# Optimization experiments

Hardware: AMD Instinct MI355X
Metric: run time of the kernel (lower is better)

Reference implementation:

```python
import jax, jax.numpy as jnp
import numpy as np

N, Q, E, D = 100000, 128, 500000, 32
D4 = 4 * D
RATIO_UPDATE = 0.2
NEG_SLOPE = 0.01  # LeakyReLU default


def setup_inputs() -> dict:
    key = jax.random.key(0)
    ks = jax.random.split(key, 16)
    return {
        "visited_node_score": jax.random.uniform(ks[0], (N,), jnp.float32),
        "node_repr": jax.random.normal(ks[1], (N, D), jnp.float32),
        "eg0": jnp.sort(jax.random.randint(ks[2], (E,), 0, Q)),
        "src0": jax.random.randint(ks[3], (E,), 0, N),
        "dst0": jax.random.randint(ks[4], (E,), 0, N),
        "rel0": jax.random.normal(ks[5], (E, D), jnp.float32),
        "eg1": jnp.sort(jax.random.randint(ks[6], (E,), 0, Q)),
        "src1": jax.random.randint(ks[7], (E,), 0, N),
        "dst1": jax.random.randint(ks[8], (E,), 0, N),
        "rel1": jax.random.normal(ks[9], (E, D), jnp.float32),
        "query_src_emb": jax.random.normal(ks[10], (Q, D), jnp.float32),
        "query_rel_emb": jax.random.normal(ks[11], (Q, D), jnp.float32),
        "Wq": jax.random.normal(ks[12], (D4, D4), jnp.float32) * np.sqrt(2.0 / D4).astype(np.float32),
        "Wk": jax.random.normal(ks[13], (D4, D4), jnp.float32) * np.sqrt(2.0 / D4).astype(np.float32),
        "Wlin": jax.random.normal(ks[14], (D, D), jnp.float32) * np.sqrt(2.0 / (2 * D)).astype(np.float32),
        "blin": jnp.zeros((D,), jnp.float32),
        "max_edges": 500,
    }


def segment_softmax(logits, seg, num_segments):
    # softmax within groups of identical seg id (source node index)
    m = jax.ops.segment_max(logits, seg, num_segments=num_segments)
    ex = jnp.exp(logits - m[seg])
    s = jax.ops.segment_sum(ex, seg, num_segments=num_segments)
    return ex / s[seg]


def segment_topk_mask(values, seg, k):
    # keep mask for per-segment top-k (seg must be sorted); stable -> first occurrence on ties
    n = values.shape[0]
    order = jnp.lexsort((-values, seg))  # primary: seg, secondary: descending value
    seg_sorted = seg[order]
    idx = jnp.arange(n)
    is_start = jnp.concatenate([jnp.array([True]), seg_sorted[1:] != seg_sorted[:-1]])
    seg_start = jax.lax.cummax(jnp.where(is_start, idx, 0))
    rank_sorted = idx - seg_start  # rank within segment, 0 = largest
    rank = jnp.zeros((n,), jnp.int32).at[order].set(rank_sorted.astype(jnp.int32))
    return rank < k


def reference(visited_node_score, node_repr, eg0, src0, dst0, rel0,
              eg1, src1, dst1, rel1, query_src_emb, query_rel_emb,
              Wq, Wk, Wlin, blin, max_edges):
    def att_logits(repr_, src, dst, eg, rel):
        q = query_src_emb[eg]
        r = query_rel_emb[eg]
        left = jnp.concatenate([repr_[src], rel, q, r], axis=-1)   # [E, 4D]
        right = jnp.concatenate([repr_[dst], rel, q, r], axis=-1)  # [E, 4D]
        return jnp.sum((left @ Wq.T) * (right @ Wk.T), axis=-1)    # [E]

    num_nodes = node_repr.shape[0]

    # ---- last layer: attention + segmented top-k pruning ----
    logits1 = att_logits(node_repr, src1, dst1, eg1, rel1)
    w1 = segment_softmax(logits1, src1, num_nodes)           # softmax over out-edges of each src node
    src_score = visited_node_score[src1]
    target_score = w1 * src_score
    keep = segment_topk_mask(target_score, eg1, max_edges)   # top-k per eg_idx
    w1p = jnp.where(keep, w1, 0.0)

    # node score aggregation == 'sum': score[n] = sum_{kept e: dst=n} w * src_score
    updated_node_score = jax.ops.segment_sum(w1p * src_score, dst1, num_segments=num_nodes)

    # representation update along pruned edges (linear_act=False)
    agg = jax.ops.segment_sum(w1p[:, None] * node_repr[src1], dst1, num_segments=num_nodes)
    repr_ = (1.0 - RATIO_UPDATE) * agg + RATIO_UPDATE * node_repr

    # ---- earlier layer(s), no pruning ----
    logits0 = att_logits(repr_, src0, dst0, eg0, rel0)
    w0 = segment_softmax(logits0, src0, num_nodes)
    agg0 = jax.ops.segment_sum(w0[:, None] * repr_[src0], dst0, num_segments=num_nodes)
    repr_ = (1.0 - RATIO_UPDATE) * agg0 + RATIO_UPDATE * repr_

    # bypass_forward: LeakyReLU(Linear(repr))
    h = repr_ @ Wlin.T + blin
    updated_repr = jnp.where(h >= 0, h, NEG_SLOPE * h)
    return updated_node_score, updated_repr
```

## Files before the change

kernel.cpp:

```cpp
#include <hip/hip_runtime.h>
#include <math.h>

#define DD 32
#define DD4 128
#define TPB 256
#define LDSCAP 6144
#define CANDCAP 2048

__device__ __forceinline__ unsigned long long dsort_key(double x) {
  unsigned long long b = (unsigned long long)__double_as_longlong(x);
  return (b & 0x8000000000000000ull) ? ~b : (b | 0x8000000000000000ull);
}
__device__ __forceinline__ double dunsort_key(unsigned long long k) {
  unsigned long long b = (k & 0x8000000000000000ull) ? (k ^ 0x8000000000000000ull) : ~k;
  return __longlong_as_double((long long)b);
}
__device__ __forceinline__ unsigned int fsort_key(float x) {
  unsigned int b = __float_as_uint(x);
  return (b & 0x80000000u) ? ~b : (b | 0x80000000u);
}
__device__ __forceinline__ float funsort_key(unsigned int k) {
  unsigned int b = (k & 0x80000000u) ? (k ^ 0x80000000u) : ~k;
  return __uint_as_float(b);
}

__device__ __forceinline__ int block_iscan256(int x, int* wsum) {
  const int lane = threadIdx.x & 63, w = threadIdx.x >> 6;
#pragma unroll
  for (int o = 1; o < 64; o <<= 1) {
    int y = __shfl_up(x, o, 64);
    if (lane >= o) x += y;
  }
  if (lane == 63) wsum[w] = x;
  __syncthreads();
  int add = 0;
#pragma unroll
  for (int i = 0; i < 4; ++i) add += (i < w) ? wsum[i] : 0;
  __syncthreads();
  return x + add;
}

__global__ __launch_bounds__(TPB) void k_precompute_M(
    const float* __restrict__ Wq, const float* __restrict__ Wk,
    double* __restrict__ M64, float* __restrict__ M32) {
  int t = blockIdx.x * blockDim.x + threadIdx.x;
  int i = t >> 7, j = t & 127;
  double acc = 0.0;
  for (int k = 0; k < DD4; ++k)
    acc += (double)Wq[k * DD4 + i] * (double)Wk[k * DD4 + j];
  M64[i * DD4 + j] = acc;
  M32[i * DD4 + j] = (float)acc;
}

__global__ __launch_bounds__(TPB) void k_sym22(
    const double* __restrict__ M64, double* __restrict__ S64, float* __restrict__ S32) {
  int i = blockIdx.x * blockDim.x + threadIdx.x;
  int r = i >> 5, c = i & 31;
  double g  = M64[(32 + r) * DD4 + 32 + c];
  double gt = M64[(32 + c) * DD4 + 32 + r];
  double s = (c > r) ? (g + gt) : ((c == r) ? g : 0.0);
  S64[i] = s;
  S32[i] = (float)s;
}

__global__ __launch_bounds__(64) void k_per_query(
    const double* __restrict__ M64,
    const float* __restrict__ qemb, const float* __restrict__ remb,
    double* __restrict__ p64, double* __restrict__ pD64, double* __restrict__ c64,
    float* __restrict__ p32, float* __restrict__ pD32, float* __restrict__ c32) {
  int q = blockIdx.x;
  int l = threadIdx.x;
  __shared__ double qr[64];
  qr[l] = (l < DD) ? (double)qemb[q * DD + l] : (double)remb[q * DD + (l - DD)];
  __syncthreads();
  double a = 0.0;
  for (int j = 0; j < 64; ++j) a += M64[l * DD4 + 64 + j] * qr[j];
  double ct = 0.0;
  for (int j = 0; j < 64; ++j) ct += M64[(64 + j) * DD4 + l] * qr[j];
  if (l >= DD) a += ct;
  p64[q * 64 + l] = a;
  p32[q * 64 + l] = (float)a;
  if (l < DD) {
    pD64[q * DD + l] = ct;
    pD32[q * DD + l] = (float)ct;
  }
  double a3 = 0.0;
  for (int j = 0; j < 64; ++j) a3 += M64[(64 + l) * DD4 + 64 + j] * qr[j];
  a3 *= qr[l];
  for (int o = 32; o; o >>= 1) a3 += __shfl_xor(a3, o);
  if (l == 0) { c64[q] = a3; c32[q] = (float)a3; }
}

#define G_T(c) Mmat[(c) * DD4 + j]
#define G_U(c) Mmat[j * DD4 + 32 + (c)]
#define G_V(c) Mmat[(32 + (c)) * DD4 + j]

#define NP_TILE(GEXPR)                                                          \
  for (int tt = 0; tt < 4; ++tt) {                                              \
    T a0=(T)0,a1=(T)0,a2=(T)0,a3=(T)0,a4=(T)0,a5=(T)0,a6=(T)0,a7=(T)0;          \
    const int c0 = tt * 8;                                                      \
    _Pragma("unroll")                                                           \
    for (int j = 0; j < 32; ++j) {                                              \
      const T hj = hh[j];                                                       \
      a0 += (GEXPR(c0 + 0)) * hj; a1 += (GEXPR(c0 + 1)) * hj;                   \
      a2 += (GEXPR(c0 + 2)) * hj; a3 += (GEXPR(c0 + 3)) * hj;                   \
      a4 += (GEXPR(c0 + 4)) * hj; a5 += (GEXPR(c0 + 5)) * hj;                   \
      a6 += (GEXPR(c0 + 6)) * hj; a7 += (GEXPR(c0 + 7)) * hj;                   \
    }                                                                           \
    xq[tid * 9 + tt * 2]     = make_float4((float)a0,(float)a1,(float)a2,(float)a3); \
    xq[tid * 9 + tt * 2 + 1] = make_float4((float)a4,(float)a5,(float)a6,(float)a7); \
  }

#define NP_STORE(dst)                                                           \
  __syncthreads();                                                              \
  {                                                                             \
    float4* go = (float4*)(dst) + (size_t)nbase * 8;                            \
    _Pragma("unroll")                                                           \
    for (int k = 0; k < 8; ++k) {                                               \
      int f = k * TPB + tid;                                                    \
      if ((f >> 3) < nlim) go[f] = xq[(f >> 3) * 9 + (f & 7)];                  \
    }                                                                           \
  }                                                                             \
  __syncthreads();

template <typename T, bool MIX>
__global__ __launch_bounds__(TPB) void k_node_pre(
    const T* __restrict__ Mmat, const float* __restrict__ reprIn,
    const float* __restrict__ aggIn, float* __restrict__ reprOut,
    float* __restrict__ t, float* __restrict__ u, float* __restrict__ v, int N_) {
  __shared__ float xp[TPB * 36];
  float4* xq = (float4*)xp;
  const int tid = threadIdx.x;
  const int nbase = blockIdx.x * TPB;
  const int n = nbase + tid;
  const int nlim = min(TPB, N_ - nbase);
  const bool valid = tid < nlim;
  T hh[32];
  if (valid) {
    const float4* h4 = (const float4*)reprIn + (size_t)n * 8;
#pragma unroll
    for (int jq = 0; jq < 8; ++jq) {
      float4 x = h4[jq];
      if constexpr (MIX) {
        const float4 a = ((const float4*)aggIn)[(size_t)n * 8 + jq];
        x = make_float4(0.8f * a.x + 0.2f * x.x, 0.8f * a.y + 0.2f * x.y,
                        0.8f * a.z + 0.2f * x.z, 0.8f * a.w + 0.2f * x.w);
        xq[tid * 9 + jq] = x;
      }
      hh[4 * jq]     = (T)x.x; hh[4 * jq + 1] = (T)x.y;
      hh[4 * jq + 2] = (T)x.z; hh[4 * jq + 3] = (T)x.w;
    }
  } else {
#pragma unroll
    for (int j = 0; j < 32; ++j) hh[j] = (T)0;
  }
  if constexpr (MIX) {
    NP_STORE(reprOut)
  }
  NP_TILE(G_T)
  NP_STORE(t)
  NP_TILE(G_U)
  NP_STORE(u)
  NP_TILE(G_V)
  NP_STORE(v)
}

template <typename T>
__global__ __launch_bounds__(TPB) void k_quad(
    const T* __restrict__ Smat,
    const float* __restrict__ rel, const int* __restrict__ eg,
    const T* __restrict__ pq, const T* __restrict__ cq,
    T* __restrict__ quad, int E) {
  const int e = blockIdx.x * TPB + threadIdx.x;
  if (e >= E) return;
  const int q = eg[e];
  T rl[32];
  {
    const float4* r4 = (const float4*)rel + (size_t)e * 8;
#pragma unroll
    for (int j = 0; j < 8; ++j) {
      float4 x = r4[j];
      rl[4 * j] = (T)x.x; rl[4 * j + 1] = (T)x.y;
      rl[4 * j + 2] = (T)x.z; rl[4 * j + 3] = (T)x.w;
    }
  }
  const T* prow = pq + (size_t)q * 64 + 32;
  T lin0 = (T)0, lin1 = (T)0;
#pragma unroll
  for (int i = 0; i < 32; i += 2) {
    lin0 += prow[i] * rl[i];
    lin1 += prow[i + 1] * rl[i + 1];
  }
  T a0 = cq[q] + lin0, a1 = lin1, a2 = (T)0, a3 = (T)0;
#pragma unroll
  for (int i = 0; i < 32; ++i) {
    T r0 = Smat[i * 32 + i] * rl[i];
    T r1 = (T)0;
#pragma unroll
    for (int j = i + 1; j < 32; ++j) {
      if ((j - i) & 1) r1 += Smat[i * 32 + j] * rl[j];
      else             r0 += Smat[i * 32 + j] * rl[j];
    }
    T rr = (r0 + r1) * rl[i];
    if ((i & 3) == 0) a0 += rr;
    else if ((i & 3) == 1) a1 += rr;
    else if ((i & 3) == 2) a2 += rr;
    else a3 += rr;
  }
  quad[e] = (a0 + a1) + (a2 + a3);
}

template <typename T>
__global__ __launch_bounds__(TPB) void k_edge_dots(
    const float* __restrict__ repr, const float* __restrict__ rel,
    const int* __restrict__ src, const int* __restrict__ dst, const int* __restrict__ eg,
    const float* __restrict__ tvec, const float* __restrict__ uvec, const float* __restrict__ vvec,
    const T* __restrict__ pq, const T* __restrict__ pDq, const T* __restrict__ quad,
    T* __restrict__ logits, void* __restrict__ mkey, int E) {
  const long long t = (long long)blockIdx.x * TPB + threadIdx.x;
  const int e = (int)(t >> 3), part = (int)(t & 7);
  if (e >= E) return;
  const int s = src[e], d = dst[e], q = eg[e];
  const float4 hs = ((const float4*)repr)[(size_t)s * 8 + part];
  const float4 td = ((const float4*)tvec)[(size_t)d * 8 + part];
  const float4 hd = ((const float4*)repr)[(size_t)d * 8 + part];
  const float4 rl = ((const float4*)rel)[(size_t)e * 8 + part];
  const float4 us = ((const float4*)uvec)[(size_t)s * 8 + part];
  const float4 vd = ((const float4*)vvec)[(size_t)d * 8 + part];
  const T* p  = pq  + (size_t)q * 64 + part * 4;
  const T* pD = pDq + (size_t)q * DD + part * 4;
  T a = (T)hs.x * ((T)td.x + p[0]) + (T)hs.y * ((T)td.y + p[1]) +
        (T)hs.z * ((T)td.z + p[2]) + (T)hs.w * ((T)td.w + p[3]);
  a += (T)hd.x * pD[0] + (T)hd.y * pD[1] + (T)hd.z * pD[2] + (T)hd.w * pD[3];
  a += (T)rl.x * (T)(us.x + vd.x) + (T)rl.y * (T)(us.y + vd.y) +
       (T)rl.z * (T)(us.z + vd.z) + (T)rl.w * (T)(us.w + vd.w);
  a += __shfl_xor(a, 1);
  a += __shfl_xor(a, 2);
  a += __shfl_xor(a, 4);
  if (part == 0) {
    a += quad[e];
    logits[e] = a;
    if constexpr (sizeof(T) == 8) {
      atomicMax((unsigned long long*)mkey + s, dsort_key((double)a));
    } else {
      atomicMax((unsigned int*)mkey + s, fsort_key((float)a));
    }
  }
}

__global__ __launch_bounds__(TPB) void k_expsum64(
    double* __restrict__ io, const unsigned long long* __restrict__ mkey,
    const int* __restrict__ src, double* __restrict__ ssum, int E) {
  int e = blockIdx.x * blockDim.x + threadIdx.x;
  if (e >= E) return;
  int s = src[e];
  double ex = exp(io[e] - dunsort_key(mkey[s]));
  io[e] = ex;
  atomicAdd(&ssum[s], ex);
}
__global__ __launch_bounds__(TPB) void k_expsum32h(
    float* __restrict__ io, const unsigned int* __restrict__ mkey,
    const int* __restrict__ src, const int* __restrict__ dst,
    float* __restrict__ ssum, int* __restrict__ cnt, int E) {
  int e = blockIdx.x * blockDim.x + threadIdx.x;
  if (e >= E) return;
  int s = src[e];
  float ex = expf(io[e] - funsort_key(mkey[s]));
  io[e] = ex;
  atomicAdd(&ssum[s], ex);
  atomicAdd(&cnt[dst[e]], 1);
}

__global__ __launch_bounds__(TPB) void k_weights_target(
    const double* __restrict__ ex, const double* __restrict__ ssum,
    const int* __restrict__ src, const float* __restrict__ score,
    const int* __restrict__ eg, int* __restrict__ qoff,
    float* __restrict__ w1f, unsigned int* __restrict__ tkey, int E, int Q) {
  int e = blockIdx.x * blockDim.x + threadIdx.x;
  if (e >= E) return;
  int s = src[e];
  double w = ex[e] / ssum[s];
  float wf = (float)w;
  w1f[e] = wf;
  float tgt = wf * score[s];
  tkey[e] = fsort_key(tgt);
  int cur = eg[e];
  int prev = (e == 0) ? -1 : eg[e - 1];
  for (int v = prev + 1; v <= cur; ++v) qoff[v] = e;
  if (e == E - 1) {
    for (int v = cur + 1; v <= Q; ++v) qoff[v] = E;
  }
}

__global__ __launch_bounds__(TPB) void k_topk(
    const unsigned int* __restrict__ tkey, const float* __restrict__ w1f,
    const int* __restrict__ qoff, const int* __restrict__ maxe,
    float* __restrict__ w1p, int E) {
  __shared__ unsigned int keys[LDSCAP];
  __shared__ int hist[256];
  __shared__ unsigned short cand[CANDCAP];
  __shared__ int wsum[4];
  __shared__ int sh_cnt;
  __shared__ unsigned int sh_prefix;
  __shared__ int sh_need;
  const int q = blockIdx.x;
  const int s = qoff[q], e2 = qoff[q + 1];
  const int n = e2 - s;
  const int K = maxe[0];
  if (n <= K) {
    for (int i = s + threadIdx.x; i < e2; i += TPB) w1p[i] = w1f[i];
    return;
  }
  const bool useLds = (n <= LDSCAP);
  if (useLds) {
    for (int i = threadIdx.x; i < n; i += TPB) keys[i] = tkey[s + i];
  }
  hist[threadIdx.x] = 0;
  __syncthreads();
  for (int i = threadIdx.x; i < n; i += TPB) {
    unsigned int k = useLds ? keys[i] : tkey[s + i];
    atomicAdd(&hist[k >> 24], 1);
  }
  __syncthreads();
  int need = K;
  {
    int h = hist[255 - threadIdx.x];
    int incl = block_iscan256(h, wsum);
    int excl = incl - h;
    if (incl >= need && excl < need) {
      sh_prefix = (unsigned int)(255 - threadIdx.x) << 24;
      sh_need = need - excl;
    }
  }
  __syncthreads();
  unsigned int prefix = sh_prefix;
  need = sh_need;
  const int cnt0 = hist[prefix >> 24];
  const bool compact = useLds && (cnt0 <= CANDCAP);
  if (threadIdx.x == 0) sh_cnt = 0;
  __syncthreads();
  if (compact) {
    const unsigned int d0 = prefix >> 24;
    for (int i = threadIdx.x; i < n; i += TPB) {
      if ((keys[i] >> 24) == d0) {
        int p = atomicAdd(&sh_cnt, 1);
        cand[p] = (unsigned short)i;
      }
    }
  }
  __syncthreads();
  const int ncand = compact ? sh_cnt : 0;
  for (int pass = 1; pass < 4; ++pass) {
    const int shift = 24 - 8 * pass;
    const unsigned int himask = 0xFFFFFFFFu << (shift + 8);
    hist[threadIdx.x] = 0;
    __syncthreads();
    if (compact) {
      for (int ci = threadIdx.x; ci < ncand; ci += TPB) {
        unsigned int k = keys[cand[ci]];
        if ((k & himask) == prefix) atomicAdd(&hist[(k >> shift) & 255], 1);
      }
    } else {
      for (int i = threadIdx.x; i < n; i += TPB) {
        unsigned int k = useLds ? keys[i] : tkey[s + i];
        if ((k & himask) == prefix) atomicAdd(&hist[(k >> shift) & 255], 1);
      }
    }
    __syncthreads();
    int h = hist[255 - threadIdx.x];
    int incl = block_iscan256(h, wsum);
    int excl = incl - h;
    if (incl >= need && excl < need) {
      sh_prefix = prefix | ((unsigned int)(255 - threadIdx.x) << shift);
      sh_need = need - excl;
    }
    __syncthreads();
    prefix = sh_prefix;
    need = sh_need;
    __syncthreads();
  }
  const unsigned int kth = prefix;
  const int r = need;
  const int C = (n + TPB - 1) / TPB;
  const int b0 = min(threadIdx.x * C, n);
  const int b1 = min(b0 + C, n);
  int myt = 0;
  for (int i = b0; i < b1; ++i) {
    unsigned int k = useLds ? keys[i] : tkey[s + i];
    myt += (k == kth) ? 1 : 0;
  }
  int tincl = block_iscan256(myt, wsum);
  int tiepre = tincl - myt;
  for (int i = b0; i < b1; ++i) {
    unsigned int k = useLds ? keys[i] : tkey[s + i];
    float v = 0.f;
    if (k > kth) {
      v = w1f[s + i];
    } else if (k == kth) {
      if (tiepre < r) v = w1f[s + i];
      ++tiepre;
    }
    w1p[s + i] = v;
  }
}

__global__ __launch_bounds__(TPB) void k_apply1(
    const float* __restrict__ w1p, const int* __restrict__ src, const int* __restrict__ dst,
    const float* __restrict__ repr0, const float* __restrict__ score,
    float* __restrict__ agg, float* __restrict__ score_out, int E) {
  int t = blockIdx.x * blockDim.x + threadIdx.x;
  int e = t >> 3, part = t & 7;
  if (e >= E) return;
  float w = w1p[e];
  if (w == 0.f) return;
  int sv = src[e], dv = dst[e];
  const float4 rv = ((const float4*)repr0)[sv * 8 + part];
  float* ap = agg + (size_t)dv * DD + part * 4;
  atomicAdd(ap + 0, w * rv.x);
  atomicAdd(ap + 1, w * rv.y);
  atomicAdd(ap + 2, w * rv.z);
  atomicAdd(ap + 3, w * rv.w);
  if (part == 0) atomicAdd(score_out + dv, w * score[sv]);
}

#define SCHUNK 1024
__global__ __launch_bounds__(TPB) void k_scan1(
    const int* __restrict__ cnt, int* __restrict__ off, int* __restrict__ bsum, int N_) {
  __shared__ int sd[TPB];
  const int b = blockIdx.x, t = threadIdx.x;
  const int base = b * SCHUNK + t * 4;
  int v[4];
  int s4 = 0;
#pragma unroll
  for (int k = 0; k < 4; ++k) {
    v[k] = (base + k < N_) ? cnt[base + k] : 0;
    s4 += v[k];
  }
  sd[t] = s4;
  __syncthreads();
  for (int o = 1; o < TPB; o <<= 1) {
    int x = (t >= o) ? sd[t - o] : 0;
    __syncthreads();
    sd[t] += x;
    __syncthreads();
  }
  int excl = sd[t] - s4;
  if (t == TPB - 1) bsum[b] = sd[t];
  int run = excl;
#pragma unroll
  for (int k = 0; k < 4; ++k) {
    if (base + k < N_) { off[base + k] = run; run += v[k]; }
  }
}

__global__ __launch_bounds__(TPB) void k_scan2(
    int* __restrict__ bsum, int* __restrict__ off, int nblk, int N_, int E) {
  __shared__ int wsum[4];
  if (nblk <= TPB) {
    int t = threadIdx.x;
    int x = (t < nblk) ? bsum[t] : 0;
    int orig = x;
    const int lane = t & 63, w = t >> 6;
#pragma unroll
    for (int o = 1; o < 64; o <<= 1) {
      int y = __shfl_up(x, o, 64);
      if (lane >= o) x += y;
    }
    if (lane == 63) wsum[w] = x;
    __syncthreads();
    int add = 0;
#pragma unroll
    for (int i = 0; i < 4; ++i) add += (i < w) ? wsum[i] : 0;
    x += add;
    if (t < nblk) bsum[t] = x - orig;
    if (t == 0) off[N_] = E;
  } else {
    if (threadIdx.x != 0) return;
    int run = 0;
    for (int i = 0; i < nblk; ++i) { int tmp = bsum[i]; bsum[i] = run; run += tmp; }
    off[N_] = E;
  }
}

__global__ __launch_bounds__(TPB) void k_scan3(
    int* __restrict__ off, const int* __restrict__ bsum, int* __restrict__ cursor, int N_) {
  int i = blockIdx.x * blockDim.x + threadIdx.x;
  if (i >= N_) return;
  int v = off[i] + bsum[i >> 10];
  off[i] = v;
  cursor[i] = v;
}

__global__ __launch_bounds__(TPB) void k_scatter0(
    const float* __restrict__ ex, const float* __restrict__ ssum,
    const int* __restrict__ src, const int* __restrict__ dst,
    int* __restrict__ cursor, float2* __restrict__ pk, int E) {
  int e = blockIdx.x * blockDim.x + threadIdx.x;
  if (e >= E) return;
  int s = src[e];
  float w = ex[e] / ssum[s];
  int pos = atomicAdd(&cursor[dst[e]], 1);
  pk[pos] = make_float2(w, __int_as_float(s));
}

__global__ __launch_bounds__(TPB) void k_gather_final(
    const float2* __restrict__ pk, const int* __restrict__ off,
    const float* __restrict__ repr1,
    const float* __restrict__ Wlin, const float* __restrict__ blin,
    float* __restrict__ out_repr, int N_) {
  __shared__ float WsT[DD * DD];
  __shared__ float bs[DD];
  for (int i = threadIdx.x; i < DD * DD; i += TPB) {
    int r = i >> 5, c = i & 31;
    WsT[c * DD + r] = Wlin[i];
  }
  if (threadIdx.x < DD) bs[threadIdx.x] = blin[threadIdx.x];
  __syncthreads();
  const int n = blockIdx.x * 8 + (threadIdx.x >> 5);
  const int c = threadIdx.x & 31;
  if (n >= N_) return;
  float acc = 0.f;
  const int j0 = off[n], j1 = off[n + 1];
  for (int base = j0; base < j1; base += 32) {
    const int m = min(32, j1 - base);
    float2 p = (base + c < j1) ? pk[base + c] : make_float2(0.f, 0.f);
    for (int j = 0; j < m; ++j) {
      const float wj = __shfl(p.x, j, 32);
      const int sj = __float_as_int(__shfl(p.y, j, 32));
      acc += wj * repr1[(size_t)sj * DD + c];
    }
  }
  float mix = 0.8f * acc + 0.2f * repr1[(size_t)n * DD + c];
  float o = bs[c];
#pragma unroll 8
  for (int j = 0; j < DD; ++j) {
    float mj = __shfl(mix, j, 32);
    o += WsT[j * DD + c] * mj;
  }
  out_repr[(size_t)n * DD + c] = (o >= 0.f) ? o : 0.01f * o;
}

extern "C" void kernel_launch(void* const* d_in, const int* in_sizes, int n_in,
                              void* d_out, int out_size, void* d_ws, size_t ws_size,
                              hipStream_t stream) {
  (void)n_in; (void)out_size; (void)ws_size;
  const float* score = (const float*)d_in[0];
  const float* nrepr = (const float*)d_in[1];
  const int*   eg0   = (const int*)d_in[2];
  const int*   src0  = (const int*)d_in[3];
  const int*   dst0  = (const int*)d_in[4];
  const float* rel0  = (const float*)d_in[5];
  const int*   eg1   = (const int*)d_in[6];
  const int*   src1  = (const int*)d_in[7];
  const int*   dst1  = (const int*)d_in[8];
  const float* rel1  = (const float*)d_in[9];
  const float* qemb  = (const float*)d_in[10];
  const float* remb  = (const float*)d_in[11];
  const float* Wq    = (const float*)d_in[12];
  const float* Wk    = (const float*)d_in[13];
  const float* Wlin  = (const float*)d_in[14];
  const float* blin  = (const float*)d_in[15];
  const int*   maxe  = (const int*)d_in[16];

  const int N_ = in_sizes[0];
  const int E_ = in_sizes[2];
  const int Q_ = in_sizes[10] / DD;

  char* wsc = (char*)d_ws;
  size_t off = 0;
  auto alloc = [&](size_t bytes) -> void* {
    void* p = wsc + off;
    off += (bytes + 255) & ~(size_t)255;
    return p;
  };
  double* M64  = (double*)alloc((size_t)DD4 * DD4 * 8);
  float*  M32  = (float*)alloc((size_t)DD4 * DD4 * 4);
  double* S64  = (double*)alloc((size_t)DD * DD * 8);
  float*  S32  = (float*)alloc((size_t)DD * DD * 4);
  double* p64  = (double*)alloc((size_t)Q_ * 64 * 8);
  double* pD64 = (double*)alloc((size_t)Q_ * DD * 8);
  double* c64  = (double*)alloc((size_t)Q_ * 8);
  float*  p32  = (float*)alloc((size_t)Q_ * 64 * 4);
  float*  pD32 = (float*)alloc((size_t)Q_ * DD * 4);
  float*  c32  = (float*)alloc((size_t)Q_ * 4);
  int*    qoff = (int*)alloc((size_t)(Q_ + 2) * 4);
  double* lg1  = (double*)alloc((size_t)E_ * 8);
  double* qv64 = (double*)alloc((size_t)E_ * 8);
  float*  w1f  = (float*)alloc((size_t)E_ * 4);
  unsigned int* tkey = (unsigned int*)alloc((size_t)E_ * 4);
  float*  w1p  = (float*)alloc((size_t)E_ * 4);
  float*  lg0  = (float*)alloc((size_t)E_ * 4);
  float*  repr1 = (float*)alloc((size_t)N_ * DD * 4);
  float*  tvec = (float*)alloc((size_t)N_ * DD * 4);
  float*  uvec = (float*)alloc((size_t)N_ * DD * 4);
  float*  vvec = (float*)alloc((size_t)N_ * DD * 4);
  size_t zstart = off;
  unsigned long long* mkey1 = (unsigned long long*)alloc((size_t)N_ * 8);
  double* s1   = (double*)alloc((size_t)N_ * 8);
  float*  agg  = (float*)alloc((size_t)N_ * DD * 4);
  unsigned int* mkey0 = (unsigned int*)alloc((size_t)N_ * 4);
  float*  s0   = (float*)alloc((size_t)N_ * 4);
  size_t zlen = off - zstart;

  float* qv32 = (float*)qv64;

  int* cnt    = (int*)tvec;
  int* offcsr = (int*)tvec + N_;
  int* cursor = (int*)tvec + 2 * (size_t)N_ + 64;
  int* bsum   = (int*)tvec + 3 * (size_t)N_ + 128;
  float2* pk  = (float2*)uvec;

  float* out_score = (float*)d_out;
  float* out_repr  = out_score + N_;

  hipMemsetAsync(wsc + zstart, 0, zlen, stream);
  hipMemsetAsync(d_out, 0, (size_t)N_ * 4, stream);

  k_precompute_M<<<(DD4 * DD4) / TPB, TPB, 0, stream>>>(Wq, Wk, M64, M32);
  k_sym22<<<4, TPB, 0, stream>>>(M64, S64, S32);
  k_per_query<<<Q_, 64, 0, stream>>>(M64, qemb, remb, p64, pD64, c64, p32, pD32, c32);

  const int ngrid = (N_ + TPB - 1) / TPB;
  const int egrid = (E_ + TPB - 1) / TPB;
  const int dgrid = (int)(((size_t)E_ * 8 + TPB - 1) / TPB);

  k_node_pre<double, false><<<ngrid, TPB, 0, stream>>>(M64, nrepr, nullptr, nullptr,
                                                       tvec, uvec, vvec, N_);
  k_quad<double><<<egrid, TPB, 0, stream>>>(S64, rel1, eg1, p64, c64, qv64, E_);
  k_edge_dots<double><<<dgrid, TPB, 0, stream>>>(nrepr, rel1, src1, dst1, eg1,
                                                 tvec, uvec, vvec, p64, pD64, qv64,
                                                 lg1, (void*)mkey1, E_);
  k_expsum64<<<egrid, TPB, 0, stream>>>(lg1, mkey1, src1, s1, E_);
  k_weights_target<<<egrid, TPB, 0, stream>>>(lg1, s1, src1, score, eg1, qoff,
                                              w1f, tkey, E_, Q_);
  k_topk<<<Q_, TPB, 0, stream>>>(tkey, w1f, qoff, maxe, w1p, E_);

  k_apply1<<<dgrid, TPB, 0, stream>>>(w1p, src1, dst1, nrepr, score, agg, out_score, E_);

  k_node_pre<float, true><<<ngrid, TPB, 0, stream>>>(M32, nrepr, agg, repr1,
                                                     tvec, uvec, vvec, N_);
  k_quad<float><<<egrid, TPB, 0, stream>>>(S32, rel0, eg0, p32, c32, qv32, E_);
  k_edge_dots<float><<<dgrid, TPB, 0, stream>>>(repr1, rel0, src0, dst0, eg0,
                                                tvec, uvec, vvec, p32, pD32, qv32,
                                                lg0, (void*)mkey0, E_);

  hipMemsetAsync(cnt, 0, (size_t)N_ * 4, stream);
  k_expsum32h<<<egrid, TPB, 0, stream>>>(lg0, mkey0, src0, dst0, s0, cnt, E_);
  const int nblk = (N_ + SCHUNK - 1) / SCHUNK;
  k_scan1<<<nblk, TPB, 0, stream>>>(cnt, offcsr, bsum, N_);
  k_scan2<<<1, TPB, 0, stream>>>(bsum, offcsr, nblk, N_, E_);
  k_scan3<<<ngrid, TPB, 0, stream>>>(offcsr, bsum, cursor, N_);
  k_scatter0<<<egrid, TPB, 0, stream>>>(lg0, s0, src0, dst0, cursor, pk, E_);
  k_gather_final<<<(N_ + 7) / 8, TPB, 0, stream>>>(pk, offcsr, repr1, Wlin, blin, out_repr, N_);
}
```

Baseline: 644.3 us.

## Process two edges per lane group and split final gather from linear layer

The edge-dot kernel now has each 8-lane group compute logits for two edges, so twice as many independent gathers are in flight per thread and half as many threads are launched. The final stage is split in two. One kernel does the CSR gather with 4-way unrolled independent loads into a mix buffer that reuses vvec. A second kernel applies the 32x32 linear layer and LeakyReLU with one node per thread, writing through shared memory via NP_STORE. The gather-side shuffles go away, at the cost of an extra N×32 buffer round trip through memory and one more launch.

```diff
diff --git a/kernel.cpp b/kernel.cpp
--- a/kernel.cpp
+++ b/kernel.cpp
@@ -218,32 +218,59 @@
     const T* __restrict__ pq, const T* __restrict__ pDq, const T* __restrict__ quad,
     T* __restrict__ logits, void* __restrict__ mkey, int E) {
   const long long t = (long long)blockIdx.x * TPB + threadIdx.x;
-  const int e = (int)(t >> 3), part = (int)(t & 7);
-  if (e >= E) return;
-  const int s = src[e], d = dst[e], q = eg[e];
-  const float4 hs = ((const float4*)repr)[(size_t)s * 8 + part];
-  const float4 td = ((const float4*)tvec)[(size_t)d * 8 + part];
-  const float4 hd = ((const float4*)repr)[(size_t)d * 8 + part];
-  const float4 rl = ((const float4*)rel)[(size_t)e * 8 + part];
-  const float4 us = ((const float4*)uvec)[(size_t)s * 8 + part];
-  const float4 vd = ((const float4*)vvec)[(size_t)d * 8 + part];
-  const T* p  = pq  + (size_t)q * 64 + part * 4;
-  const T* pD = pDq + (size_t)q * DD + part * 4;
-  T a = (T)hs.x * ((T)td.x + p[0]) + (T)hs.y * ((T)td.y + p[1]) +
-        (T)hs.z * ((T)td.z + p[2]) + (T)hs.w * ((T)td.w + p[3]);
-  a += (T)hd.x * pD[0] + (T)hd.y * pD[1] + (T)hd.z * pD[2] + (T)hd.w * pD[3];
-  a += (T)rl.x * (T)(us.x + vd.x) + (T)rl.y * (T)(us.y + vd.y) +
-       (T)rl.z * (T)(us.z + vd.z) + (T)rl.w * (T)(us.w + vd.w);
-  a += __shfl_xor(a, 1);
-  a += __shfl_xor(a, 2);
-  a += __shfl_xor(a, 4);
+  const int part = (int)(t & 7);
+  const int e0 = (int)((t >> 3) * 2);
+  if (e0 >= E) return;
+  const int e1 = e0 + 1;
+  const bool has1 = (e1 < E);
+  const int s0 = src[e0], d0 = dst[e0], q0 = eg[e0];
+  const int s1 = has1 ? src[e1] : s0;
+  const int d1 = has1 ? dst[e1] : d0;
+  const int q1 = has1 ? eg[e1] : q0;
+  const float4* R  = (const float4*)repr;
+  const float4* Tv = (const float4*)tvec;
+  const float4* Uv = (const float4*)uvec;
+  const float4* Vv = (const float4*)vvec;
+  const float4* RL = (const float4*)rel;
+  const float4 hs0 = R[(size_t)s0 * 8 + part],  hs1 = R[(size_t)s1 * 8 + part];
+  const float4 td0 = Tv[(size_t)d0 * 8 + part], td1 = Tv[(size_t)d1 * 8 + part];
+  const float4 hd0 = R[(size_t)d0 * 8 + part],  hd1 = R[(size_t)d1 * 8 + part];
+  const float4 us0 = Uv[(size_t)s0 * 8 + part], us1 = Uv[(size_t)s1 * 8 + part];
+  const float4 vd0 = Vv[(size_t)d0 * 8 + part], vd1 = Vv[(size_t)d1 * 8 + part];
+  const float4 rl0 = RL[(size_t)e0 * 8 + part];
+  const float4 rl1 = has1 ? RL[(size_t)e1 * 8 + part] : rl0;
+  const T* p0  = pq  + (size_t)q0 * 64 + part * 4;
+  const T* p1  = pq  + (size_t)q1 * 64 + part * 4;
+  const T* pD0 = pDq + (size_t)q0 * DD + part * 4;
+  const T* pD1 = pDq + (size_t)q1 * DD + part * 4;
+  T a = (T)hs0.x * ((T)td0.x + p0[0]) + (T)hs0.y * ((T)td0.y + p0[1]) +
+        (T)hs0.z * ((T)td0.z + p0[2]) + (T)hs0.w * ((T)td0.w + p0[3]);
+  a += (T)hd0.x * pD0[0] + (T)hd0.y * pD0[1] + (T)hd0.z * pD0[2] + (T)hd0.w * pD0[3];
+  a += (T)rl0.x * (T)(us0.x + vd0.x) + (T)rl0.y * (T)(us0.y + vd0.y) +
+       (T)rl0.z * (T)(us0.z + vd0.z) + (T)rl0.w * (T)(us0.w + vd0.w);
+  T b = (T)hs1.x * ((T)td1.x + p1[0]) + (T)hs1.y * ((T)td1.y + p1[1]) +
+        (T)hs1.z * ((T)td1.z + p1[2]) + (T)hs1.w * ((T)td1.w + p1[3]);
+  b += (T)hd1.x * pD1[0] + (T)hd1.y * pD1[1] + (T)hd1.z * pD1[2] + (T)hd1.w * pD1[3];
+  b += (T)rl1.x * (T)(us1.x + vd1.x) + (T)rl1.y * (T)(us1.y + vd1.y) +
+       (T)rl1.z * (T)(us1.z + vd1.z) + (T)rl1.w * (T)(us1.w + vd1.w);
+  a += __shfl_xor(a, 1); a += __shfl_xor(a, 2); a += __shfl_xor(a, 4);
+  b += __shfl_xor(b, 1); b += __shfl_xor(b, 2); b += __shfl_xor(b, 4);
   if (part == 0) {
-    a += quad[e];
-    logits[e] = a;
+    a += quad[e0];
+    logits[e0] = a;
     if constexpr (sizeof(T) == 8) {
-      atomicMax((unsigned long long*)mkey + s, dsort_key((double)a));
+      atomicMax((unsigned long long*)mkey + s0, dsort_key((double)a));
     } else {
-      atomicMax((unsigned int*)mkey + s, fsort_key((float)a));
+      atomicMax((unsigned int*)mkey + s0, fsort_key((float)a));
+    }
+    if (has1) {
+      b += quad[e1];
+      logits[e1] = b;
+      if constexpr (sizeof(T) == 8) {
+        atomicMax((unsigned long long*)mkey + s1, dsort_key((double)b));
+      } else {
+        atomicMax((unsigned int*)mkey + s1, fsort_key((float)b));
+      }
     }
   }
 }
@@ -503,41 +530,75 @@
   pk[pos] = make_float2(w, __int_as_float(s));
 }
 
-__global__ __launch_bounds__(TPB) void k_gather_final(
+__global__ __launch_bounds__(TPB) void k_gather_mix(
     const float2* __restrict__ pk, const int* __restrict__ off,
-    const float* __restrict__ repr1,
-    const float* __restrict__ Wlin, const float* __restrict__ blin,
-    float* __restrict__ out_repr, int N_) {
-  __shared__ float WsT[DD * DD];
-  __shared__ float bs[DD];
-  for (int i = threadIdx.x; i < DD * DD; i += TPB) {
-    int r = i >> 5, c = i & 31;
-    WsT[c * DD + r] = Wlin[i];
-  }
-  if (threadIdx.x < DD) bs[threadIdx.x] = blin[threadIdx.x];
-  __syncthreads();
+    const float* __restrict__ repr1, float* __restrict__ mixbuf, int N_) {
   const int n = blockIdx.x * 8 + (threadIdx.x >> 5);
   const int c = threadIdx.x & 31;
   if (n >= N_) return;
+  const float self = repr1[(size_t)n * DD + c];
   float acc = 0.f;
   const int j0 = off[n], j1 = off[n + 1];
-  for (int base = j0; base < j1; base += 32) {
-    const int m = min(32, j1 - base);
-    float2 p = (base + c < j1) ? pk[base + c] : make_float2(0.f, 0.f);
-    for (int j = 0; j < m; ++j) {
-      const float wj = __shfl(p.x, j, 32);
-      const int sj = __float_as_int(__shfl(p.y, j, 32));
-      acc += wj * repr1[(size_t)sj * DD + c];
-    }
-  }
-  float mix = 0.8f * acc + 0.2f * repr1[(size_t)n * DD + c];
-  float o = bs[c];
-#pragma unroll 8
-  for (int j = 0; j < DD; ++j) {
-    float mj = __shfl(mix, j, 32);
-    o += WsT[j * DD + c] * mj;
-  }
-  out_repr[(size_t)n * DD + c] = (o >= 0.f) ? o : 0.01f * o;
+  int j = j0;
+  for (; j + 4 <= j1; j += 4) {
+    const float2 p0 = pk[j], p1 = pk[j + 1], p2 = pk[j + 2], p3 = pk[j + 3];
+    const float g0 = repr1[(size_t)__float_as_int(p0.y) * DD + c];
+    const float g1 = repr1[(size_t)__float_as_int(p1.y) * DD + c];
+    const float g2 = repr1[(size_t)__float_as_int(p2.y) * DD + c];
+    const float g3 = repr1[(size_t)__float_as_int(p3.y) * DD + c];
+    acc += p0.x * g0;
+    acc += p1.x * g1;
+    acc += p2.x * g2;
+    acc += p3.x * g3;
+  }
+  for (; j < j1; ++j) {
+    const float2 p = pk[j];
+    acc += p.x * repr1[(size_t)__float_as_int(p.y) * DD + c];
+  }
+  mixbuf[(size_t)n * DD + c] = 0.8f * acc + 0.2f * self;
+}
+
+__global__ __launch_bounds__(TPB) void k_final_linear(
+    const float* __restrict__ Wlin, const float* __restrict__ blin,
+    const float* __restrict__ mixbuf, float* __restrict__ out_repr, int N_) {
+  __shared__ float xp[TPB * 36];
+  float4* xq = (float4*)xp;
+  const int tid = threadIdx.x;
+  const int nbase = blockIdx.x * TPB;
+  const int n = nbase + tid;
+  const int nlim = min(TPB, N_ - nbase);
+  float m[32];
+  if (tid < nlim) {
+    const float4* h4 = (const float4*)mixbuf + (size_t)n * 8;
+#pragma unroll
+    for (int jq = 0; jq < 8; ++jq) {
+      float4 x = h4[jq];
+      m[4 * jq] = x.x; m[4 * jq + 1] = x.y; m[4 * jq + 2] = x.z; m[4 * jq + 3] = x.w;
+    }
+  } else {
+#pragma unroll
+    for (int j = 0; j < 32; ++j) m[j] = 0.f;
+  }
+  for (int tt = 0; tt < 4; ++tt) {
+    const int c0 = tt * 8;
+    float a0 = blin[c0 + 0], a1 = blin[c0 + 1], a2 = blin[c0 + 2], a3 = blin[c0 + 3];
+    float a4 = blin[c0 + 4], a5 = blin[c0 + 5], a6 = blin[c0 + 6], a7 = blin[c0 + 7];
+#pragma unroll
+    for (int j = 0; j < 32; ++j) {
+      const float hj = m[j];
+      a0 += Wlin[(c0 + 0) * DD + j] * hj; a1 += Wlin[(c0 + 1) * DD + j] * hj;
+      a2 += Wlin[(c0 + 2) * DD + j] * hj; a3 += Wlin[(c0 + 3) * DD + j] * hj;
+      a4 += Wlin[(c0 + 4) * DD + j] * hj; a5 += Wlin[(c0 + 5) * DD + j] * hj;
+      a6 += Wlin[(c0 + 6) * DD + j] * hj; a7 += Wlin[(c0 + 7) * DD + j] * hj;
+    }
+    a0 = (a0 >= 0.f) ? a0 : 0.01f * a0; a1 = (a1 >= 0.f) ? a1 : 0.01f * a1;
+    a2 = (a2 >= 0.f) ? a2 : 0.01f * a2; a3 = (a3 >= 0.f) ? a3 : 0.01f * a3;
+    a4 = (a4 >= 0.f) ? a4 : 0.01f * a4; a5 = (a5 >= 0.f) ? a5 : 0.01f * a5;
+    a6 = (a6 >= 0.f) ? a6 : 0.01f * a6; a7 = (a7 >= 0.f) ? a7 : 0.01f * a7;
+    xq[tid * 9 + tt * 2]     = make_float4(a0, a1, a2, a3);
+    xq[tid * 9 + tt * 2 + 1] = make_float4(a4, a5, a6, a7);
+  }
+  NP_STORE(out_repr)
 }
 
 extern "C" void kernel_launch(void* const* d_in, const int* in_sizes, int n_in,
@@ -609,6 +670,7 @@
   int* cursor = (int*)tvec + 2 * (size_t)N_ + 64;
   int* bsum   = (int*)tvec + 3 * (size_t)N_ + 128;
   float2* pk  = (float2*)uvec;
+  float* mixbuf = vvec;
 
   float* out_score = (float*)d_out;
   float* out_repr  = out_score + N_;
@@ -622,27 +684,28 @@
 
   const int ngrid = (N_ + TPB - 1) / TPB;
   const int egrid = (E_ + TPB - 1) / TPB;
-  const int dgrid = (int)(((size_t)E_ * 8 + TPB - 1) / TPB);
+  const int dgrid1 = (int)(((size_t)E_ * 8 + TPB - 1) / TPB);
+  const int dgrid2 = (int)(((size_t)((E_ + 1) / 2) * 8 + TPB - 1) / TPB);
 
   k_node_pre<double, false><<<ngrid, TPB, 0, stream>>>(M64, nrepr, nullptr, nullptr,
                                                        tvec, uvec, vvec, N_);
   k_quad<double><<<egrid, TPB, 0, stream>>>(S64, rel1, eg1, p64, c64, qv64, E_);
-  k_edge_dots<double><<<dgrid, TPB, 0, stream>>>(nrepr, rel1, src1, dst1, eg1,
-                                                 tvec, uvec, vvec, p64, pD64, qv64,
-                                                 lg1, (void*)mkey1, E_);
+  k_edge_dots<double><<<dgrid2, TPB, 0, stream>>>(nrepr, rel1, src1, dst1, eg1,
+                                                  tvec, uvec, vvec, p64, pD64, qv64,
+                                                  lg1, (void*)mkey1, E_);
   k_expsum64<<<egrid, TPB, 0, stream>>>(lg1, mkey1, src1, s1, E_);
   k_weights_target<<<egrid, TPB, 0, stream>>>(lg1, s1, src1, score, eg1, qoff,
                                               w1f, tkey, E_, Q_);
   k_topk<<<Q_, TPB, 0, stream>>>(tkey, w1f, qoff, maxe, w1p, E_);
 
-  k_apply1<<<dgrid, TPB, 0, stream>>>(w1p, src1, dst1, nrepr, score, agg, out_score, E_);
+  k_apply1<<<dgrid1, TPB, 0, stream>>>(w1p, src1, dst1, nrepr, score, agg, out_score, E_);
 
   k_node_pre<float, true><<<ngrid, TPB, 0, stream>>>(M32, nrepr, agg, repr1,
                                                      tvec, uvec, vvec, N_);
   k_quad<float><<<egrid, TPB, 0, stream>>>(S32, rel0, eg0, p32, c32, qv32, E_);
-  k_edge_dots<float><<<dgrid, TPB, 0, stream>>>(repr1, rel0, src0, dst0, eg0,
-                                                tvec, uvec, vvec, p32, pD32, qv32,
-                                                lg0, (void*)mkey0, E_);
+  k_edge_dots<float><<<dgrid2, TPB, 0, stream>>>(repr1, rel0, src0, dst0, eg0,
+                                                 tvec, uvec, vvec, p32, pD32, qv32,
+                                                 lg0, (void*)mkey0, E_);
 
   hipMemsetAsync(cnt, 0, (size_t)N_ * 4, stream);
   k_expsum32h<<<egrid, TPB, 0, stream>>>(lg0, mkey0, src0, dst0, s0, cnt, E_);
@@ -651,5 +714,6 @@
   k_scan2<<<1, TPB, 0, stream>>>(bsum, offcsr, nblk, N_, E_);
   k_scan3<<<ngrid, TPB, 0, stream>>>(offcsr, bsum, cursor, N_);
   k_scatter0<<<egrid, TPB, 0, stream>>>(lg0, s0, src0, dst0, cursor, pk, E_);
-  k_gather_final<<<(N_ + 7) / 8, TPB, 0, stream>>>(pk, offcsr, repr1, Wlin, blin, out_repr, N_);
-}
+  k_gather_mix<<<(N_ + 7) / 8, TPB, 0, stream>>>(pk, offcsr, repr1, mixbuf, N_);
+  k_final_linear<<<ngrid, TPB, 0, stream>>>(Wlin, blin, mixbuf, out_repr, N_);
+}
```

New measurement: 623.4 us. -3.3%, faster.
